# Kernel tuning notes

Measured on AMD Instinct MI355X. Metric: run time of the kernel, lower is better.

## Reference

```python
import jax, jax.numpy as jnp
import numpy as np

B, NA, F, K, L = 96, 48, 128, 64, 6
CUT = 5.0


def _forward(pos, f_in, emb, msg_w1, msg_b1, msg_w2, msg_b2, rbf_w, rbf_b,
             upd_U, upd_V, upd_w1, upd_b1, upd_w2, upd_b2,
             out_w1, out_b1, out_w2, out_b2, node_atom):
    p = pos.reshape(B, NA, 3)
    rij = p[:, :, None, :] - p[:, None, :, :]          # [B,n,n,3], pos_i - pos_j
    d2 = jnp.sum(rij * rij, -1)
    eye = jnp.eye(NA, dtype=bool)
    d = jnp.sqrt(jnp.where(eye, 1.0, d2))              # safe sqrt on diagonal
    mask = (~eye) & (d < CUT)                          # radius_graph, loop=False
    centers = jnp.linspace(0.0, CUT, K)
    gamma = 1.0 / ((CUT / K) ** 2 + 1e-9)
    rbf = jnp.exp(-gamma * (d[..., None] - centers) ** 2)   # [B,n,n,K]
    cutf = 0.5 * (jnp.cos(jnp.pi * d / CUT) + 1.0)          # cosine cutoff
    w_env = jnp.where(mask, cutf, 0.0)[..., None]
    dirv = rij / d[..., None]                               # unit directions
    s = emb[node_atom].reshape(B, NA, F)
    v = jnp.zeros((B, NA, 3, F), s.dtype)
    for l in range(L):
        # message block
        phi = jax.nn.silu(s @ msg_w1[l] + msg_b1[l]) @ msg_w2[l] + msg_b2[l]  # [B,n,3F]
        Wf = (rbf @ rbf_w[l] + rbf_b[l]) * w_env                              # [B,n,n,3F]
        x = phi[:, None, :, :] * Wf                                           # phi of sender j
        ds, dvv, dvs = jnp.split(x, 3, axis=-1)
        s = s + ds.sum(2)
        v = v + jnp.einsum('bijf,bjcf->bicf', dvv, v) \
              + jnp.einsum('bijf,bijc->bicf', dvs, dirv)
        # update block
        Uv = jnp.einsum('bncf,fg->bncg', v, upd_U[l])
        Vv = jnp.einsum('bncf,fg->bncg', v, upd_V[l])
        Vn = jnp.sqrt(jnp.sum(Vv * Vv, 2) + 1e-8)                             # [B,n,F]
        a = jax.nn.silu(jnp.concatenate([s, Vn], -1) @ upd_w1[l] + upd_b1[l]) @ upd_w2[l] + upd_b2[l]
        avv, asv, ass = jnp.split(a, 3, -1)
        v = v + avv[:, :, None, :] * Uv
        s = s + asv * jnp.sum(Uv * Vv, 2) + ass
    out = jax.nn.silu(s @ out_w1 + out_b1) @ out_w2 + out_b2                  # [B,n,1]
    return out.sum(1)                                                         # per-graph sum


def setup_inputs() -> dict:
    key = jax.random.key(0)
    ks = jax.random.split(key, 16)
    N = B * NA
    pos = jax.random.normal(ks[0], (N, 3), jnp.float32) * 2.0
    f_in = jnp.zeros((N, 1), jnp.float32)
    node_atom = jax.random.randint(ks[1], (N,), 1, 84)
    batch = jnp.arange(N) // NA
    g = lambda k, shp, fan: jax.random.normal(k, shp, jnp.float32) / np.sqrt(fan)
    return dict(
        f_in=f_in, pos=pos, batch=batch, node_atom=node_atom,
        emb=g(ks[2], (100, F), 1.0),
        msg_w1=g(ks[3], (L, F, F), F), msg_b1=jnp.zeros((L, F), jnp.float32),
        msg_w2=g(ks[4], (L, F, 3 * F), F), msg_b2=jnp.zeros((L, 3 * F), jnp.float32),
        rbf_w=g(ks[5], (L, K, 3 * F), K), rbf_b=jnp.zeros((L, 3 * F), jnp.float32),
        upd_U=g(ks[6], (L, F, F), F), upd_V=g(ks[7], (L, F, F), F),
        upd_w1=g(ks[8], (L, 2 * F, F), 2 * F), upd_b1=jnp.zeros((L, F), jnp.float32),
        upd_w2=g(ks[9], (L, F, 3 * F), F), upd_b2=jnp.zeros((L, 3 * F), jnp.float32),
        out_w1=g(ks[10], (F, F), F), out_b1=jnp.zeros((F,), jnp.float32),
        out_w2=g(ks[11], (F, 1), F), out_b2=jnp.zeros((1,), jnp.float32),
    )


def reference(f_in, pos, batch, node_atom, emb, msg_w1, msg_b1, msg_w2, msg_b2,
              rbf_w, rbf_b, upd_U, upd_V, upd_w1, upd_b1, upd_w2, upd_b2,
              out_w1, out_b1, out_w2, out_b2):
    return _forward(pos, f_in, emb, msg_w1, msg_b1, msg_w2, msg_b2, rbf_w, rbf_b,
                    upd_U, upd_V, upd_w1, upd_b1, upd_w2, upd_b2,
                    out_w1, out_b1, out_w2, out_b2, node_atom)
```

## Files before the change

kernel.cpp:

```cpp
#include <hip/hip_runtime.h>
#include <math.h>

#define NB 96
#define NA 48
#define NF 128
#define NK 64
#define NL 6
#define NN (NB*NA)
#define F3 (3*NF)
#define CUTF 5.0f
#define GAMMA_F ((float)(1.0 / (0.006103515625 + 1e-9)))
#define PI_F 3.14159265358979323846f

typedef __attribute__((ext_vector_type(8))) short short8;
typedef __attribute__((ext_vector_type(4))) float floatx4;
typedef __attribute__((ext_vector_type(2))) float floatx2;

#define LO2(v) __builtin_shufflevector(v, v, 0, 1)
#define HI2(v) __builtin_shufflevector(v, v, 2, 3)

__device__ __forceinline__ float silu_f(float x) { return x / (1.0f + expf(-x)); }

__device__ __forceinline__ short f2bf(float x) {
    unsigned u = __builtin_bit_cast(unsigned, x);
    unsigned r = (u + 0x7fffu + ((u >> 16) & 1u)) >> 16;
    return (short)r;
}
__device__ __forceinline__ float bf2f(short h) {
    unsigned u = ((unsigned)(unsigned short)h) << 16;
    return __builtin_bit_cast(float, u);
}
__device__ __forceinline__ floatx4 mfma1(short8 a, short8 b, floatx4 c) {
    return __builtin_amdgcn_mfma_f32_16x16x32_bf16(a, b, c, 0, 0, 0);
}
__device__ __forceinline__ floatx4 mfma3(short8 ah, short8 al, short8 bh, short8 bl, floatx4 c) {
    c = __builtin_amdgcn_mfma_f32_16x16x32_bf16(ah, bh, c, 0, 0, 0);
    c = __builtin_amdgcn_mfma_f32_16x16x32_bf16(al, bh, c, 0, 0, 0);
    c = __builtin_amdgcn_mfma_f32_16x16x32_bf16(ah, bl, c, 0, 0, 0);
    return c;
}

__global__ void prep_kernel(const float* __restrict__ msg_w1, const float* __restrict__ msg_w2,
                            const float* __restrict__ rbf_w, const float* __restrict__ upd_U,
                            const float* __restrict__ upd_V, const float* __restrict__ upd_w1,
                            const float* __restrict__ upd_w2,
                            short* w1T_h, short* w1T_l, short* w2T_h, short* w2T_l,
                            short* rbfT_h, short* rbfT_l, short* UT_h, short* UT_l,
                            short* VT_h, short* VT_l, short* u1T_h, short* u1T_l,
                            short* u2T_h, short* u2T_l) {
    int m = blockIdx.y;
    int l = blockIdx.x / 384;
    int n = blockIdx.x % 384;
    const float* src; short* dh; short* dl; int K, N;
    switch (m) {
      case 0: src = msg_w1; dh = w1T_h; dl = w1T_l; K = NF;   N = NF; break;
      case 1: src = msg_w2; dh = w2T_h; dl = w2T_l; K = NF;   N = F3; break;
      case 2: src = rbf_w;  dh = rbfT_h;dl = rbfT_l;K = NK;   N = F3; break;
      case 3: src = upd_U;  dh = UT_h;  dl = UT_l;  K = NF;   N = NF; break;
      case 4: src = upd_V;  dh = VT_h;  dl = VT_l;  K = NF;   N = NF; break;
      case 5: src = upd_w1; dh = u1T_h; dl = u1T_l; K = 2*NF; N = NF; break;
      default:src = upd_w2; dh = u2T_h; dl = u2T_l; K = NF;   N = F3; break;
    }
    if (n >= N) return;
    for (int k = threadIdx.x; k < K; k += 64) {
        float x = src[((size_t)l*K + k)*N + n];
        short h = f2bf(x);
        size_t off = (size_t)l*N*K
                   + (size_t)((((n>>4)*(K>>5) + (k>>5))*4 + ((k>>3)&3))*128 + (n&15)*8 + (k&7));
        dh[off] = h;
        dl[off] = f2bf(x - bf2f(h));
    }
}

__global__ void __launch_bounds__(256) geom_kernel(const float* __restrict__ pos,
                                                   float* __restrict__ dG,
                                                   float* __restrict__ weG,
                                                   float* __restrict__ dirG) {
    int e = blockIdx.x*256 + threadIdx.x;
    int i = e / NA, j = e % NA;
    int b = i / NA, il = i % NA;
    int jg = b*NA + j;
    float dx = pos[i*3+0] - pos[jg*3+0];
    float dy = pos[i*3+1] - pos[jg*3+1];
    float dz = pos[i*3+2] - pos[jg*3+2];
    float d2 = dx*dx + dy*dy + dz*dz;
    float dd = sqrtf((j == il) ? 1.0f : d2);
    bool valid = (j != il) && (dd < CUTF);
    float we = valid ? 0.5f*(cosf(PI_F * dd / CUTF) + 1.0f) : 0.0f;
    dG[e] = dd;
    weG[e] = we;
    float inv = 1.0f / dd;
    dirG[0*(size_t)NN*NA + e] = dx*inv;
    dirG[1*(size_t)NN*NA + e] = dy*inv;
    dirG[2*(size_t)NN*NA + e] = dz*inv;
}

__global__ void zero_kernel(float* __restrict__ p) {
    p[(size_t)blockIdx.x * blockDim.x + threadIdx.x] = 0.f;
}

__global__ void __launch_bounds__(128) init_phi_kernel(
        const float* __restrict__ emb, const int* __restrict__ node_atom,
        const short* __restrict__ w1T_h, const short* __restrict__ w1T_l,
        const float* __restrict__ b1,
        const short* __restrict__ w2T_h, const short* __restrict__ w2T_l,
        const float* __restrict__ b2,
        float* __restrict__ s, float* __restrict__ v, float* __restrict__ phiT) {
    __shared__ short sH[16*NF], sL[16*NF];
    __shared__ short hH[16*NF], hL[16*NF];
    int t = threadIdx.x;
    int w = t >> 6, lane = t & 63, quad = lane >> 4, col = lane & 15;
    int n0 = blockIdx.x * 16;
    for (int e = t; e < 16*NF; e += 128) {
        int n = e >> 7, f = e & 127;
        int a = node_atom[n0+n];
        float x = emb[(size_t)a*NF + f];
        s[(size_t)(n0+n)*NF + f] = x;
        short h = f2bf(x);
        int ad = n*NF + (((f >> 3) ^ (n & 7)) << 3) + (f & 7);
        sH[ad] = h; sL[ad] = f2bf(x - bf2f(h));
    }
    for (int e = t; e < 16*F3; e += 128) v[(size_t)n0*F3 + e] = 0.f;
    __syncthreads();
    #pragma unroll
    for (int nt = 0; nt < 4; ++nt) {
        int fh = w*64 + nt*16 + col;
        floatx4 acc = (floatx4){0.f,0.f,0.f,0.f};
        #pragma unroll
        for (int ks = 0; ks < 4; ++ks) {
            int ad = col*NF + (((ks*4 + quad) ^ (col & 7)) << 3);
            size_t off = (size_t)((((w*4 + nt)*4 + ks)*4 + quad)*128) + col*8;
            acc = mfma3(*(short8*)&sH[ad], *(short8*)&sL[ad],
                        *(const short8*)(w1T_h + off), *(const short8*)(w1T_l + off), acc);
        }
        float bias = b1[fh];
        #pragma unroll
        for (int r = 0; r < 4; ++r) {
            int n = quad*4 + r;
            float hv = silu_f(acc[r] + bias);
            short h = f2bf(hv);
            int ad = n*NF + (((fh >> 3) ^ (n & 7)) << 3) + (fh & 7);
            hH[ad] = h; hL[ad] = f2bf(hv - bf2f(h));
        }
    }
    __syncthreads();
    #pragma unroll
    for (int nt = 0; nt < 12; ++nt) {
        int tt = w*192 + nt*16 + col;
        floatx4 acc = (floatx4){0.f,0.f,0.f,0.f};
        #pragma unroll
        for (int ks = 0; ks < 4; ++ks) {
            int ad = col*NF + (((ks*4 + quad) ^ (col & 7)) << 3);
            size_t off = (size_t)((((w*12 + nt)*4 + ks)*4 + quad)*128) + col*8;
            acc = mfma3(*(short8*)&hH[ad], *(short8*)&hL[ad],
                        *(const short8*)(w2T_h + off), *(const short8*)(w2T_l + off), acc);
        }
        float bias = b2[tt];
        floatx4 o;
        #pragma unroll
        for (int r = 0; r < 4; ++r) o[r] = acc[r] + bias;
        *(floatx4*)(phiT + (size_t)tt*NN + n0 + quad*4) = o;
    }
}

__global__ void __launch_bounds__(512, 2) message_kernel(
        const float* __restrict__ sIn, const float* __restrict__ vIn,
        const float* __restrict__ phiT, const float* __restrict__ vT,
        const float* __restrict__ dG, const float* __restrict__ weG,
        const float* __restrict__ dirG,
        const short* __restrict__ rbfT_h,
        const float* __restrict__ rbf_b_l,
        float* __restrict__ sOut, float* __restrict__ vOut) {
    __shared__ short tkL[36*512];
    __shared__ float weL[6][NA];
    __shared__ float dirL[3][6][NA];
    int raw = blockIdx.x;
    int xcd = raw & 7, idx = raw >> 3;
    int graph = xcd + 8*(idx % 12);
    int itile = idx / 12;
    int i0l = itile*6, jbase = graph*NA;
    int n0 = jbase + i0l;
    int t = threadIdx.x;
    int w = t >> 6, lane = t & 63, quad = lane >> 4, col = lane & 15;
    int f = w*16 + col;
    float rb0 = rbf_b_l[f], rb1 = rbf_b_l[NF+f], rb2 = rbf_b_l[2*NF+f];
    floatx2 rb0v = {rb0, rb0}, rb1v = {rb1, rb1}, rb2v = {rb2, rb2};
    short8 B[3][2];
    #pragma unroll
    for (int g = 0; g < 3; ++g)
        #pragma unroll
        for (int ks = 0; ks < 2; ++ks)
            B[g][ks] = *(const short8*)(rbfT_h + (size_t)((((g*8 + w)*2 + ks)*4 + quad)*128) + col*8);
    for (int u = t; u < 576; u += 512) {
        int p = u >> 1, half = u & 1;
        int ii = p / NA, j = p % NA;
        int i = n0 + ii;
        float dd = dG[(size_t)i*NA + j];
        float we = weG[(size_t)i*NA + j];
        if (half == 0) {
            weL[ii][j] = we;
            dirL[0][ii][j] = dirG[0*(size_t)NN*NA + (size_t)i*NA + j];
            dirL[1][ii][j] = dirG[1*(size_t)NN*NA + (size_t)i*NA + j];
            dirL[2][ii][j] = dirG[2*(size_t)NN*NA + (size_t)i*NA + j];
        }
        int mt = j >> 4, colj = j & 15;
        int base = ((ii*3 + mt)*2 + half) << 9;
        #pragma unroll
        for (int c = 0; c < 4; ++c) {
            short8 h8;
            #pragma unroll
            for (int kk = 0; kk < 8; ++kk) {
                int k = half*32 + c*8 + kk;
                float cen = CUTF * (float)k / 63.0f;
                float df = dd - cen;
                h8[kk] = f2bf(__expf(-GAMMA_F * df * df) * we);
            }
            *(short8*)&tkL[base + (c*16 + colj)*8] = h8;
        }
    }
    __syncthreads();
    float accS[6], av0[6], av1[6], av2[6];
    #pragma unroll
    for (int ia = 0; ia < 6; ++ia) { accS[ia]=0.f; av0[ia]=0.f; av1[ia]=0.f; av2[ia]=0.f; }
    #pragma unroll 1
    for (int mt = 0; mt < 3; ++mt) {
        int jq = jbase + mt*16 + quad*4;
        floatx4 p0 = *(const floatx4*)(phiT + (size_t)f*NN + jq);
        floatx4 p1 = *(const floatx4*)(phiT + (size_t)(NF+f)*NN + jq);
        floatx4 p2 = *(const floatx4*)(phiT + (size_t)(2*NF+f)*NN + jq);
        floatx4 u0 = *(const floatx4*)(vT + (size_t)(0*NF+f)*NN + jq);
        floatx4 u1 = *(const floatx4*)(vT + (size_t)(1*NF+f)*NN + jq);
        floatx4 u2 = *(const floatx4*)(vT + (size_t)(2*NF+f)*NN + jq);
        int jl = mt*16 + quad*4;
        #pragma unroll
        for (int ia = 0; ia < 6; ++ia) {
            floatx4 C0 = (floatx4){0.f,0.f,0.f,0.f};
            floatx4 C1 = (floatx4){0.f,0.f,0.f,0.f};
            floatx4 C2 = (floatx4){0.f,0.f,0.f,0.f};
            #pragma unroll
            for (int ks = 0; ks < 2; ++ks) {
                short8 a = *(short8*)&tkL[(((ia*3 + mt)*2 + ks) << 9) + lane*8];
                C0 = mfma1(a, B[0][ks], C0);
                C1 = mfma1(a, B[1][ks], C1);
                C2 = mfma1(a, B[2][ks], C2);
            }
            floatx4 we4 = *(const floatx4*)&weL[ia][jl];
            floatx4 d0 = *(const floatx4*)&dirL[0][ia][jl];
            floatx4 d1 = *(const floatx4*)&dirL[1][ia][jl];
            floatx4 d2 = *(const floatx4*)&dirL[2][ia][jl];
            floatx2 aS = {0.f,0.f}, a0 = {0.f,0.f}, a1 = {0.f,0.f}, a2 = {0.f,0.f};
            {
                floatx2 we2 = LO2(we4);
                floatx2 Wf0 = rb0v*we2 + LO2(C0);
                aS += LO2(p0) * Wf0;
                floatx2 Wf1 = rb1v*we2 + LO2(C1);
                floatx2 x1 = LO2(p1) * Wf1;
                a0 += x1 * LO2(u0);
                a1 += x1 * LO2(u1);
                a2 += x1 * LO2(u2);
                floatx2 Wf2 = rb2v*we2 + LO2(C2);
                floatx2 x2 = LO2(p2) * Wf2;
                a0 += x2 * LO2(d0);
                a1 += x2 * LO2(d1);
                a2 += x2 * LO2(d2);
            }
            {
                floatx2 we2 = HI2(we4);
                floatx2 Wf0 = rb0v*we2 + HI2(C0);
                aS += HI2(p0) * Wf0;
                floatx2 Wf1 = rb1v*we2 + HI2(C1);
                floatx2 x1 = HI2(p1) * Wf1;
                a0 += x1 * HI2(u0);
                a1 += x1 * HI2(u1);
                a2 += x1 * HI2(u2);
                floatx2 Wf2 = rb2v*we2 + HI2(C2);
                floatx2 x2 = HI2(p2) * Wf2;
                a0 += x2 * HI2(d0);
                a1 += x2 * HI2(d1);
                a2 += x2 * HI2(d2);
            }
            accS[ia] += aS.x + aS.y;
            av0[ia]  += a0.x + a0.y;
            av1[ia]  += a1.x + a1.y;
            av2[ia]  += a2.x + a2.y;
        }
    }
    #pragma unroll
    for (int ia = 0; ia < 6; ++ia) {
        int i = n0 + ia;
        float aS = accS[ia], A0 = av0[ia], A1 = av1[ia], A2 = av2[ia];
        aS += __shfl_xor(aS, 16, 64); aS += __shfl_xor(aS, 32, 64);
        A0 += __shfl_xor(A0, 16, 64); A0 += __shfl_xor(A0, 32, 64);
        A1 += __shfl_xor(A1, 16, 64); A1 += __shfl_xor(A1, 32, 64);
        A2 += __shfl_xor(A2, 16, 64); A2 += __shfl_xor(A2, 32, 64);
        if (quad == 0) {
            sOut[(size_t)i*NF + f]        = sIn[(size_t)i*NF + f]        + aS;
            vOut[(size_t)i*F3 + f]        = vIn[(size_t)i*F3 + f]        + A0;
            vOut[(size_t)i*F3 + NF + f]   = vIn[(size_t)i*F3 + NF + f]   + A1;
            vOut[(size_t)i*F3 + 2*NF + f] = vIn[(size_t)i*F3 + 2*NF + f] + A2;
        }
    }
}

__global__ void __launch_bounds__(512) update_phi_kernel(
        const short* __restrict__ UT_h, const short* __restrict__ VT_h,
        const short* __restrict__ u1T_h, const float* __restrict__ b1,
        const short* __restrict__ u2T_h, const float* __restrict__ b2,
        float* __restrict__ s, float* __restrict__ v, float* __restrict__ vT,
        int doPhi,
        const short* __restrict__ pw1_h, const float* __restrict__ pb1,
        const short* __restrict__ pw2_h, const float* __restrict__ pb2,
        float* __restrict__ phiT) {
    __shared__ short A1h[48*NF], A1l[48*NF];
    __shared__ short A2h[16*256];
    __shared__ short hH[16*NF];
    __shared__ float sF[6*132];
    int t = threadIdx.x;
    int w = t >> 6, lane = t & 63, quad = lane >> 4, col = lane & 15;
    int raw = blockIdx.x;
    int xcd = raw & 7, idx = raw >> 3;
    int graph = xcd + 8*(idx % 12);
    int n0 = graph*NA + (idx / 12)*6;
    int f = w*16 + col;
    for (int e = t; e < 6*F3; e += 512) {
        int n = e / F3, cf = e % F3;
        int c = cf >> 7, ff = cf & 127;
        float x = v[(size_t)(n0+n)*F3 + cf];
        int row = c*16 + n;
        short h = f2bf(x);
        int ad = row*NF + (((ff >> 3) ^ (row & 7)) << 3) + (ff & 7);
        A1h[ad] = h; A1l[ad] = f2bf(x - bf2f(h));
    }
    for (int e = t; e < 6*NF; e += 512) {
        int n = e >> 7, ff = e & 127;
        float x = s[(size_t)(n0+n)*NF + ff];
        sF[n*132 + ff] = x;
        int ad = n*256 + (((ff >> 3) ^ (n & 7)) << 3) + (ff & 7);
        A2h[ad] = f2bf(x);
    }
    __syncthreads();
    floatx4 Uacc[3], Vacc[3];
    #pragma unroll
    for (int mt = 0; mt < 3; ++mt) { Uacc[mt] = (floatx4){0.f,0.f,0.f,0.f}; Vacc[mt] = (floatx4){0.f,0.f,0.f,0.f}; }
    #pragma unroll
    for (int ks = 0; ks < 4; ++ks) {
        size_t off = (size_t)(((w*4 + ks)*4 + quad)*128) + col*8;
        short8 BU = *(const short8*)(UT_h + off);
        short8 BV = *(const short8*)(VT_h + off);
        #pragma unroll
        for (int mt = 0; mt < 3; ++mt) {
            int row = mt*16 + col;
            int ad = row*NF + (((ks*4 + quad) ^ (row & 7)) << 3);
            short8 ah = *(short8*)&A1h[ad];
            Uacc[mt] = mfma1(ah, BU, Uacc[mt]);
            Vacc[mt] = mfma1(ah, BV, Vacc[mt]);
        }
    }
    if (quad < 2) {
        #pragma unroll
        for (int r = 0; r < 4; ++r) {
            int n = quad*4 + r;
            if (n < 6) {
                float v0 = Vacc[0][r], v1 = Vacc[1][r], v2 = Vacc[2][r];
                float vn = sqrtf(v0*v0 + v1*v1 + v2*v2 + 1e-8f);
                int ad = n*256 + ((((128 + f) >> 3) ^ (n & 7)) << 3) + (f & 7);
                A2h[ad] = f2bf(vn);
            }
        }
    }
    __syncthreads();
    {
        floatx4 H = (floatx4){0.f,0.f,0.f,0.f};
        #pragma unroll
        for (int ks = 0; ks < 8; ++ks) {
            int ad = col*256 + (((ks*4 + quad) ^ (col & 7)) << 3);
            short8 ah = *(short8*)&A2h[ad];
            size_t off = (size_t)(((w*8 + ks)*4 + quad)*128) + col*8;
            H = mfma1(ah, *(const short8*)(u1T_h + off), H);
        }
        float bias = b1[f];
        if (quad < 2) {
            #pragma unroll
            for (int r = 0; r < 4; ++r) {
                int n = quad*4 + r;
                if (n < 6) {
                    float hv = silu_f(H[r] + bias);
                    int ad = n*NF + (((f >> 3) ^ (n & 7)) << 3) + (f & 7);
                    hH[ad] = f2bf(hv);
                }
            }
        }
    }
    __syncthreads();
    floatx4 O[3];
    #pragma unroll
    for (int gg = 0; gg < 3; ++gg) O[gg] = (floatx4){0.f,0.f,0.f,0.f};
    #pragma unroll
    for (int ks = 0; ks < 4; ++ks) {
        int ad = col*NF + (((ks*4 + quad) ^ (col & 7)) << 3);
        short8 ah = *(short8*)&hH[ad];
        #pragma unroll
        for (int gg = 0; gg < 3; ++gg) {
            size_t off = (size_t)((((gg*8 + w)*4 + ks)*4 + quad)*128) + col*8;
            O[gg] = mfma1(ah, *(const short8*)(u2T_h + off), O[gg]);
        }
    }
    __syncthreads();
    short* pH = A2h;
    if (quad < 2) {
        float bavv = b2[f], basv = b2[NF + f], bass = b2[2*NF + f];
        #pragma unroll
        for (int r = 0; r < 4; ++r) {
            int n = quad*4 + r;
            if (n < 6) {
                float avv = O[0][r] + bavv;
                float asv = O[1][r] + basv;
                float ass = O[2][r] + bass;
                float dot = Uacc[0][r]*Vacc[0][r] + Uacc[1][r]*Vacc[1][r] + Uacc[2][r]*Vacc[2][r];
                float snew = sF[n*132 + f] + asv*dot + ass;
                s[(size_t)(n0+n)*NF + f] = snew;
                int adS = n*NF + (((f >> 3) ^ (n & 7)) << 3) + (f & 7);
                pH[adS] = f2bf(snew);
                #pragma unroll
                for (int c = 0; c < 3; ++c) {
                    int row = c*16 + n;
                    int ad = row*NF + (((f >> 3) ^ (row & 7)) << 3) + (f & 7);
                    float vold = bf2f(A1h[ad]) + bf2f(A1l[ad]);
                    float vnew = vold + avv*Uacc[c][r];
                    v[(size_t)(n0+n)*F3 + c*NF + f] = vnew;
                    vT[(size_t)(c*NF + f)*NN + n0 + n] = vnew;
                }
            }
        }
    }
    if (!doPhi) return;
    __syncthreads();
    {
        floatx4 acc = (floatx4){0.f,0.f,0.f,0.f};
        #pragma unroll
        for (int ks = 0; ks < 4; ++ks) {
            int ad = col*NF + (((ks*4 + quad) ^ (col & 7)) << 3);
            size_t off = (size_t)(((w*4 + ks)*4 + quad)*128) + col*8;
            acc = mfma1(*(short8*)&pH[ad], *(const short8*)(pw1_h + off), acc);
        }
        float bias = pb1[f];
        if (quad < 2) {
            #pragma unroll
            for (int r = 0; r < 4; ++r) {
                int n = quad*4 + r;
                if (n < 6) {
                    float hv = silu_f(acc[r] + bias);
                    int ad = n*NF + (((f >> 3) ^ (n & 7)) << 3) + (f & 7);
                    hH[ad] = f2bf(hv);
                }
            }
        }
    }
    __syncthreads();
    #pragma unroll
    for (int nt = 0; nt < 3; ++nt) {
        int tt = (w*3 + nt)*16 + col;
        floatx4 acc = (floatx4){0.f,0.f,0.f,0.f};
        #pragma unroll
        for (int ks = 0; ks < 4; ++ks) {
            int ad = col*NF + (((ks*4 + quad) ^ (col & 7)) << 3);
            size_t off = (size_t)((((w*3 + nt)*4 + ks)*4 + quad)*128) + col*8;
            acc = mfma1(*(short8*)&hH[ad], *(const short8*)(pw2_h + off), acc);
        }
        float bias = pb2[tt];
        if (quad == 0) {
            floatx4 o;
            #pragma unroll
            for (int r = 0; r < 4; ++r) o[r] = acc[r] + bias;
            *(floatx4*)(phiT + (size_t)tt*NN + n0) = o;
        } else if (quad == 1) {
            floatx2 o2 = { acc[0] + bias, acc[1] + bias };
            *(floatx2*)(phiT + (size_t)tt*NN + n0 + 4) = o2;
        }
    }
}

__global__ void zero_out_kernel(float* __restrict__ out) {
    out[threadIdx.x] = 0.f;
}

__global__ void out_kernel(const float* __restrict__ s,
                           const float* __restrict__ w1, const float* __restrict__ b1,
                           const float* __restrict__ w2, const float* __restrict__ b2,
                           float* __restrict__ out) {
    int n = blockIdx.x;
    int f = threadIdx.x;
    __shared__ float sh[NF];
    __shared__ float r2[2];
    sh[f] = s[n*NF + f];
    __syncthreads();
    float acc = b1[f];
    for (int g = 0; g < NF; ++g) acc = fmaf(sh[g], w1[g*NF + f], acc);
    float p = silu_f(acc) * w2[f];
    #pragma unroll
    for (int off = 32; off > 0; off >>= 1) p += __shfl_down(p, off, 64);
    if ((f & 63) == 0) r2[f >> 6] = p;
    __syncthreads();
    if (f == 0) atomicAdd(&out[n / NA], r2[0] + r2[1] + b2[0]);
}

extern "C" void kernel_launch(void* const* d_in, const int* in_sizes, int n_in,
                              void* d_out, int out_size, void* d_ws, size_t ws_size,
                              hipStream_t stream) {
    (void)in_sizes; (void)n_in; (void)out_size; (void)ws_size;
    const float* pos      = (const float*)d_in[1];
    const int*   node_atom= (const int*)  d_in[3];
    const float* emb      = (const float*)d_in[4];
    const float* msg_w1   = (const float*)d_in[5];
    const float* msg_b1   = (const float*)d_in[6];
    const float* msg_w2   = (const float*)d_in[7];
    const float* msg_b2   = (const float*)d_in[8];
    const float* rbf_w    = (const float*)d_in[9];
    const float* rbf_b    = (const float*)d_in[10];
    const float* upd_U    = (const float*)d_in[11];
    const float* upd_V    = (const float*)d_in[12];
    const float* upd_w1   = (const float*)d_in[13];
    const float* upd_b1   = (const float*)d_in[14];
    const float* upd_w2   = (const float*)d_in[15];
    const float* upd_b2   = (const float*)d_in[16];
    const float* out_w1   = (const float*)d_in[17];
    const float* out_b1   = (const float*)d_in[18];
    const float* out_w2   = (const float*)d_in[19];
    const float* out_b2   = (const float*)d_in[20];
    float* out = (float*)d_out;

    float* ws   = (float*)d_ws;
    float* sA   = ws; ws += (size_t)NN*NF;
    float* sB   = ws; ws += (size_t)NN*NF;
    float* vA   = ws; ws += (size_t)NN*F3;
    float* vB   = ws; ws += (size_t)NN*F3;
    float* phiT = ws; ws += (size_t)F3*NN;
    float* vT   = ws; ws += (size_t)F3*NN;
    float* dG   = ws; ws += (size_t)NN*NA;
    float* weG  = ws; ws += (size_t)NN*NA;
    float* dirG = ws; ws += (size_t)3*NN*NA;
    short* sp    = (short*)ws;
    short* w1T_h = sp; sp += (size_t)NL*NF*NF;
    short* w1T_l = sp; sp += (size_t)NL*NF*NF;
    short* w2T_h = sp; sp += (size_t)NL*F3*NF;
    short* w2T_l = sp; sp += (size_t)NL*F3*NF;
    short* rbfT_h= sp; sp += (size_t)NL*F3*NK;
    short* rbfT_l= sp; sp += (size_t)NL*F3*NK;
    short* UT_h  = sp; sp += (size_t)NL*NF*NF;
    short* UT_l  = sp; sp += (size_t)NL*NF*NF;
    short* VT_h  = sp; sp += (size_t)NL*NF*NF;
    short* VT_l  = sp; sp += (size_t)NL*NF*NF;
    short* u1T_h = sp; sp += (size_t)NL*NF*2*NF;
    short* u1T_l = sp; sp += (size_t)NL*NF*2*NF;
    short* u2T_h = sp; sp += (size_t)NL*F3*NF;
    short* u2T_l = sp; sp += (size_t)NL*F3*NF;

    prep_kernel<<<dim3(NL*384, 7), 64, 0, stream>>>(msg_w1, msg_w2, rbf_w, upd_U, upd_V, upd_w1, upd_w2,
                                                    w1T_h, w1T_l, w2T_h, w2T_l, rbfT_h, rbfT_l,
                                                    UT_h, UT_l, VT_h, VT_l, u1T_h, u1T_l, u2T_h, u2T_l);
    geom_kernel<<<(NN*NA)/256, 256, 0, stream>>>(pos, dG, weG, dirG);
    zero_kernel<<<(F3*NN)/256, 256, 0, stream>>>(vT);
    init_phi_kernel<<<NN/16, 128, 0, stream>>>(emb, node_atom,
                                               w1T_h, w1T_l, msg_b1, w2T_h, w2T_l, msg_b2,
                                               sA, vA, phiT);

    float* sC = sA; float* vC = vA; float* sN = sB; float* vN = vB;
    for (int l = 0; l < NL; ++l) {
        message_kernel<<<NB*8, 512, 0, stream>>>(sC, vC, phiT, vT,
                                                 dG, weG, dirG,
                                                 rbfT_h + (size_t)l*F3*NK,
                                                 rbf_b + (size_t)l*F3, sN, vN);
        int lp = (l + 1 < NL) ? (l + 1) : 0;
        update_phi_kernel<<<NN/6, 512, 0, stream>>>(
            UT_h + (size_t)l*NF*NF, VT_h + (size_t)l*NF*NF,
            u1T_h + (size_t)l*NF*2*NF, upd_b1 + (size_t)l*NF,
            u2T_h + (size_t)l*F3*NF, upd_b2 + (size_t)l*F3,
            sN, vN, vT,
            (l + 1 < NL) ? 1 : 0,
            w1T_h + (size_t)lp*NF*NF, msg_b1 + (size_t)lp*NF,
            w2T_h + (size_t)lp*F3*NF, msg_b2 + (size_t)lp*F3,
            phiT);
        float* tp;
        tp = sC; sC = sN; sN = tp;
        tp = vC; vC = vN; vN = tp;
    }
    zero_out_kernel<<<1, NB, 0, stream>>>(out);
    out_kernel<<<NN, NF, 0, stream>>>(sC, out_w1, out_b1, out_w2, out_b2, out);
}
```

Before: 562.0 us.

## Precompute packed RBF tiles once in geom kernel and regroup phi/v layout per graph

The bf16 RBF×envelope tiles were recomputed with exp calls in every message-kernel launch (six layers). They are now computed once in the geometry kernel, stored in a packed global buffer, and copied into LDS with vector loads. The phi and v transposed buffers are also reorganised into a per-graph, per-16-node-tile layout so the message kernel reads contiguous chunks. The cost is extra global memory traffic (about 27 MB of packed RBF read per layer) and scattered scalar stores in the update kernel.

```diff
diff --git a/kernel.cpp b/kernel.cpp
--- a/kernel.cpp
+++ b/kernel.cpp
@@ -18,6 +18,8 @@
 
 #define LO2(v) __builtin_shufflevector(v, v, 0, 1)
 #define HI2(v) __builtin_shufflevector(v, v, 2, 3)
+
+#define PHX(g, mt, ff, jl) (((((size_t)(g))*3 + (mt))*384 + (ff))*16 + (jl))
 
 __device__ __forceinline__ float silu_f(float x) { return x / (1.0f + expf(-x)); }
 
@@ -73,9 +75,9 @@
 }
 
 __global__ void __launch_bounds__(256) geom_kernel(const float* __restrict__ pos,
-                                                   float* __restrict__ dG,
                                                    float* __restrict__ weG,
-                                                   float* __restrict__ dirG) {
+                                                   float* __restrict__ dirG,
+                                                   short* __restrict__ rbfP) {
     int e = blockIdx.x*256 + threadIdx.x;
     int i = e / NA, j = e % NA;
     int b = i / NA, il = i % NA;
@@ -87,12 +89,28 @@
     float dd = sqrtf((j == il) ? 1.0f : d2);
     bool valid = (j != il) && (dd < CUTF);
     float we = valid ? 0.5f*(cosf(PI_F * dd / CUTF) + 1.0f) : 0.0f;
-    dG[e] = dd;
     weG[e] = we;
     float inv = 1.0f / dd;
     dirG[0*(size_t)NN*NA + e] = dx*inv;
     dirG[1*(size_t)NN*NA + e] = dy*inv;
     dirG[2*(size_t)NN*NA + e] = dz*inv;
+    int mt = j >> 4, colj = j & 15;
+    size_t rb = (size_t)i*3072 + (size_t)(mt*2)*512 + (size_t)colj*8;
+    #pragma unroll
+    for (int half = 0; half < 2; ++half) {
+        #pragma unroll
+        for (int c = 0; c < 4; ++c) {
+            short8 h8;
+            #pragma unroll
+            for (int kk = 0; kk < 8; ++kk) {
+                int k = half*32 + c*8 + kk;
+                float cen = CUTF * (float)k / 63.0f;
+                float df = dd - cen;
+                h8[kk] = f2bf(__expf(-GAMMA_F * df * df) * we);
+            }
+            *(short8*)&rbfP[rb + half*512 + c*128] = h8;
+        }
+    }
 }
 
 __global__ void zero_kernel(float* __restrict__ p) {
@@ -105,12 +123,13 @@
         const float* __restrict__ b1,
         const short* __restrict__ w2T_h, const short* __restrict__ w2T_l,
         const float* __restrict__ b2,
-        float* __restrict__ s, float* __restrict__ v, float* __restrict__ phiT) {
+        float* __restrict__ s, float* __restrict__ v, float* __restrict__ phiX) {
     __shared__ short sH[16*NF], sL[16*NF];
     __shared__ short hH[16*NF], hL[16*NF];
     int t = threadIdx.x;
     int w = t >> 6, lane = t & 63, quad = lane >> 4, col = lane & 15;
     int n0 = blockIdx.x * 16;
+    int g = n0 / NA, mt0 = (n0 % NA) >> 4;
     for (int e = t; e < 16*NF; e += 128) {
         int n = e >> 7, f = e & 127;
         int a = node_atom[n0+n];
@@ -159,15 +178,15 @@
         floatx4 o;
         #pragma unroll
         for (int r = 0; r < 4; ++r) o[r] = acc[r] + bias;
-        *(floatx4*)(phiT + (size_t)tt*NN + n0 + quad*4) = o;
+        *(floatx4*)(phiX + PHX(g, mt0, tt, quad*4)) = o;
     }
 }
 
 __global__ void __launch_bounds__(512, 2) message_kernel(
         const float* __restrict__ sIn, const float* __restrict__ vIn,
-        const float* __restrict__ phiT, const float* __restrict__ vT,
-        const float* __restrict__ dG, const float* __restrict__ weG,
-        const float* __restrict__ dirG,
+        const float* __restrict__ phiX, const float* __restrict__ vX,
+        const float* __restrict__ weG, const float* __restrict__ dirG,
+        const short* __restrict__ rbfP,
         const short* __restrict__ rbfT_h,
         const float* __restrict__ rbf_b_l,
         float* __restrict__ sOut, float* __restrict__ vOut) {
@@ -191,31 +210,17 @@
         #pragma unroll
         for (int ks = 0; ks < 2; ++ks)
             B[g][ks] = *(const short8*)(rbfT_h + (size_t)((((g*8 + w)*2 + ks)*4 + quad)*128) + col*8);
-    for (int u = t; u < 576; u += 512) {
-        int p = u >> 1, half = u & 1;
-        int ii = p / NA, j = p % NA;
-        int i = n0 + ii;
-        float dd = dG[(size_t)i*NA + j];
-        float we = weG[(size_t)i*NA + j];
-        if (half == 0) {
-            weL[ii][j] = we;
-            dirL[0][ii][j] = dirG[0*(size_t)NN*NA + (size_t)i*NA + j];
-            dirL[1][ii][j] = dirG[1*(size_t)NN*NA + (size_t)i*NA + j];
-            dirL[2][ii][j] = dirG[2*(size_t)NN*NA + (size_t)i*NA + j];
-        }
-        int mt = j >> 4, colj = j & 15;
-        int base = ((ii*3 + mt)*2 + half) << 9;
-        #pragma unroll
-        for (int c = 0; c < 4; ++c) {
-            short8 h8;
-            #pragma unroll
-            for (int kk = 0; kk < 8; ++kk) {
-                int k = half*32 + c*8 + kk;
-                float cen = CUTF * (float)k / 63.0f;
-                float df = dd - cen;
-                h8[kk] = f2bf(__expf(-GAMMA_F * df * df) * we);
-            }
-            *(short8*)&tkL[base + (c*16 + colj)*8] = h8;
+    {
+        const short8* rs = (const short8*)(rbfP + (size_t)n0*3072);
+        short8* rd = (short8*)tkL;
+        for (int u = t; u < 2304; u += 512) rd[u] = rs[u];
+        if (t < 288) {
+            int ii = t / NA, j = t % NA;
+            size_t e = (size_t)(n0 + ii)*NA + j;
+            weL[ii][j] = weG[e];
+            dirL[0][ii][j] = dirG[0*(size_t)NN*NA + e];
+            dirL[1][ii][j] = dirG[1*(size_t)NN*NA + e];
+            dirL[2][ii][j] = dirG[2*(size_t)NN*NA + e];
         }
     }
     __syncthreads();
@@ -224,13 +229,13 @@
     for (int ia = 0; ia < 6; ++ia) { accS[ia]=0.f; av0[ia]=0.f; av1[ia]=0.f; av2[ia]=0.f; }
     #pragma unroll 1
     for (int mt = 0; mt < 3; ++mt) {
-        int jq = jbase + mt*16 + quad*4;
-        floatx4 p0 = *(const floatx4*)(phiT + (size_t)f*NN + jq);
-        floatx4 p1 = *(const floatx4*)(phiT + (size_t)(NF+f)*NN + jq);
-        floatx4 p2 = *(const floatx4*)(phiT + (size_t)(2*NF+f)*NN + jq);
-        floatx4 u0 = *(const floatx4*)(vT + (size_t)(0*NF+f)*NN + jq);
-        floatx4 u1 = *(const floatx4*)(vT + (size_t)(1*NF+f)*NN + jq);
-        floatx4 u2 = *(const floatx4*)(vT + (size_t)(2*NF+f)*NN + jq);
+        int jq = quad*4;
+        floatx4 p0 = *(const floatx4*)(phiX + PHX(graph, mt, f, jq));
+        floatx4 p1 = *(const floatx4*)(phiX + PHX(graph, mt, NF+f, jq));
+        floatx4 p2 = *(const floatx4*)(phiX + PHX(graph, mt, 2*NF+f, jq));
+        floatx4 u0 = *(const floatx4*)(vX + PHX(graph, mt, 0*NF+f, jq));
+        floatx4 u1 = *(const floatx4*)(vX + PHX(graph, mt, 1*NF+f, jq));
+        floatx4 u2 = *(const floatx4*)(vX + PHX(graph, mt, 2*NF+f, jq));
         int jl = mt*16 + quad*4;
         #pragma unroll
         for (int ia = 0; ia < 6; ++ia) {
@@ -306,11 +311,11 @@
         const short* __restrict__ UT_h, const short* __restrict__ VT_h,
         const short* __restrict__ u1T_h, const float* __restrict__ b1,
         const short* __restrict__ u2T_h, const float* __restrict__ b2,
-        float* __restrict__ s, float* __restrict__ v, float* __restrict__ vT,
+        float* __restrict__ s, float* __restrict__ v, float* __restrict__ vX,
         int doPhi,
         const short* __restrict__ pw1_h, const float* __restrict__ pb1,
         const short* __restrict__ pw2_h, const float* __restrict__ pb2,
-        float* __restrict__ phiT) {
+        float* __restrict__ phiX) {
     __shared__ short A1h[48*NF], A1l[48*NF];
     __shared__ short A2h[16*256];
     __shared__ short hH[16*NF];
@@ -320,7 +325,8 @@
     int raw = blockIdx.x;
     int xcd = raw & 7, idx = raw >> 3;
     int graph = xcd + 8*(idx % 12);
-    int n0 = graph*NA + (idx / 12)*6;
+    int jb0 = (idx / 12)*6;
+    int n0 = graph*NA + jb0;
     int f = w*16 + col;
     for (int e = t; e < 6*F3; e += 512) {
         int n = e / F3, cf = e % F3;
@@ -421,6 +427,8 @@
                 s[(size_t)(n0+n)*NF + f] = snew;
                 int adS = n*NF + (((f >> 3) ^ (n & 7)) << 3) + (f & 7);
                 pH[adS] = f2bf(snew);
+                int jl = jb0 + n;
+                int mtt = jl >> 4, jl16 = jl & 15;
                 #pragma unroll
                 for (int c = 0; c < 3; ++c) {
                     int row = c*16 + n;
@@ -428,7 +436,7 @@
                     float vold = bf2f(A1h[ad]) + bf2f(A1l[ad]);
                     float vnew = vold + avv*Uacc[c][r];
                     v[(size_t)(n0+n)*F3 + c*NF + f] = vnew;
-                    vT[(size_t)(c*NF + f)*NN + n0 + n] = vnew;
+                    vX[PHX(graph, mtt, c*NF + f, jl16)] = vnew;
                 }
             }
         }
@@ -468,14 +476,16 @@
             acc = mfma1(*(short8*)&hH[ad], *(const short8*)(pw2_h + off), acc);
         }
         float bias = pb2[tt];
-        if (quad == 0) {
-            floatx4 o;
+        if (quad < 2) {
             #pragma unroll
-            for (int r = 0; r < 4; ++r) o[r] = acc[r] + bias;
-            *(floatx4*)(phiT + (size_t)tt*NN + n0) = o;
-        } else if (quad == 1) {
-            floatx2 o2 = { acc[0] + bias, acc[1] + bias };
-            *(floatx2*)(phiT + (size_t)tt*NN + n0 + 4) = o2;
+            for (int r = 0; r < 4; ++r) {
+                int no = quad*4 + r;
+                if (no < 6) {
+                    int jl = jb0 + no;
+                    int mtt = jl >> 4, jl16 = jl & 15;
+                    phiX[PHX(graph, mtt, tt, jl16)] = acc[r] + bias;
+                }
+            }
         }
     }
 }
@@ -534,12 +544,12 @@
     float* sB   = ws; ws += (size_t)NN*NF;
     float* vA   = ws; ws += (size_t)NN*F3;
     float* vB   = ws; ws += (size_t)NN*F3;
-    float* phiT = ws; ws += (size_t)F3*NN;
-    float* vT   = ws; ws += (size_t)F3*NN;
-    float* dG   = ws; ws += (size_t)NN*NA;
+    float* phiX = ws; ws += (size_t)F3*NN;
+    float* vX   = ws; ws += (size_t)F3*NN;
     float* weG  = ws; ws += (size_t)NN*NA;
     float* dirG = ws; ws += (size_t)3*NN*NA;
     short* sp    = (short*)ws;
+    short* rbfP  = sp; sp += (size_t)NN*3072;
     short* w1T_h = sp; sp += (size_t)NL*NF*NF;
     short* w1T_l = sp; sp += (size_t)NL*NF*NF;
     short* w2T_h = sp; sp += (size_t)NL*F3*NF;
@@ -558,16 +568,16 @@
     prep_kernel<<<dim3(NL*384, 7), 64, 0, stream>>>(msg_w1, msg_w2, rbf_w, upd_U, upd_V, upd_w1, upd_w2,
                                                     w1T_h, w1T_l, w2T_h, w2T_l, rbfT_h, rbfT_l,
                                                     UT_h, UT_l, VT_h, VT_l, u1T_h, u1T_l, u2T_h, u2T_l);
-    geom_kernel<<<(NN*NA)/256, 256, 0, stream>>>(pos, dG, weG, dirG);
-    zero_kernel<<<(F3*NN)/256, 256, 0, stream>>>(vT);
+    geom_kernel<<<(NN*NA)/256, 256, 0, stream>>>(pos, weG, dirG, rbfP);
+    zero_kernel<<<(F3*NN)/256, 256, 0, stream>>>(vX);
     init_phi_kernel<<<NN/16, 128, 0, stream>>>(emb, node_atom,
                                                w1T_h, w1T_l, msg_b1, w2T_h, w2T_l, msg_b2,
-                                               sA, vA, phiT);
+                                               sA, vA, phiX);
 
     float* sC = sA; float* vC = vA; float* sN = sB; float* vN = vB;
     for (int l = 0; l < NL; ++l) {
-        message_kernel<<<NB*8, 512, 0, stream>>>(sC, vC, phiT, vT,
-                                                 dG, weG, dirG,
+        message_kernel<<<NB*8, 512, 0, stream>>>(sC, vC, phiX, vX,
+                                                 weG, dirG, rbfP,
                                                  rbfT_h + (size_t)l*F3*NK,
                                                  rbf_b + (size_t)l*F3, sN, vN);
         int lp = (l + 1 < NL) ? (l + 1) : 0;
@@ -575,11 +585,11 @@
             UT_h + (size_t)l*NF*NF, VT_h + (size_t)l*NF*NF,
             u1T_h + (size_t)l*NF*2*NF, upd_b1 + (size_t)l*NF,
             u2T_h + (size_t)l*F3*NF, upd_b2 + (size_t)l*F3,
-            sN, vN, vT,
+            sN, vN, vX,
             (l + 1 < NL) ? 1 : 0,
             w1T_h + (size_t)lp*NF*NF, msg_b1 + (size_t)lp*NF,
             w2T_h + (size_t)lp*F3*NF, msg_b2 + (size_t)lp*F3,
-            phiT);
+            phiX);
         float* tp;
         tp = sC; sC = sN; sN = tp;
         tp = vC; vC = vN; vN = tp;
```

After: 537.3 us. 4.4% less time.
